# Performance work log

Measured on AMD Instinct MI355X. Metric: run time of the kernel, lower is better.

## Reference

```python
import jax, jax.numpy as jnp
import numpy as np

B, S, D = 4, 4096, 2048
H, DH = 16, 128
ROPE_BASE = 10000.0


def rotate_half(x):
    x1, x2 = jnp.split(x, 2, axis=-1)
    return jnp.concatenate((-x2, x1), axis=-1)


def rope_cos_sin(seq_len, head_dim, dtype):
    inv_freq = 1.0 / (ROPE_BASE ** (jnp.arange(0, head_dim, 2, dtype=jnp.float32) / head_dim))
    pos = jnp.arange(seq_len, dtype=jnp.float32)
    freqs = pos[:, None] * inv_freq[None, :]          # [S, DH/2]
    emb = jnp.concatenate((freqs, freqs), axis=-1)    # [S, DH]
    return jnp.cos(emb).astype(dtype), jnp.sin(emb).astype(dtype)


def setup_inputs() -> dict:
    key = jax.random.key(0)
    ks = jax.random.split(key, 5)
    scale = 0.02
    return {
        "hidden_states": jax.random.normal(ks[0], (B, S, D), jnp.float32),
        "Wq": jax.random.normal(ks[1], (D, D), jnp.float32) * scale,
        "Wk": jax.random.normal(ks[2], (D, D), jnp.float32) * scale,
        "Wv": jax.random.normal(ks[3], (D, D), jnp.float32) * scale,
        "Wo": jax.random.normal(ks[4], (D, D), jnp.float32) * scale,
    }


def reference(hidden_states, Wq, Wk, Wv, Wo):
    b, s, d = hidden_states.shape
    # QKV projections (nn.Linear stores weight as [out, in] -> x @ W.T)
    def proj(W):
        y = hidden_states @ W.T                       # [B, S, D]
        return y.reshape(b, s, H, DH).transpose(0, 2, 1, 3)  # [B, H, S, DH]
    q, k, v = proj(Wq), proj(Wk), proj(Wv)

    # RoPE (cos/sin broadcast over head dim: unsqueeze_dim=1)
    cos, sin = rope_cos_sin(s, DH, hidden_states.dtype)  # [S, DH]
    cos = cos[None, None]                                # [1, 1, S, DH]
    sin = sin[None, None]
    q = q * cos + rotate_half(q) * sin
    k = k * cos + rotate_half(k) * sin

    # SDPA, non-causal, no mask, eval mode (dropout 0)
    scale = 1.0 / jnp.sqrt(jnp.asarray(DH, hidden_states.dtype))
    scores = jnp.einsum("bhqd,bhkd->bhqk", q, k) * scale
    attn = jax.nn.softmax(scores, axis=-1)
    ctx = jnp.einsum("bhqk,bhkd->bhqd", attn, v)         # [B, H, S, DH]

    ctx = ctx.transpose(0, 2, 1, 3).reshape(b, s, H * DH)
    return ctx @ Wo.T
```

## Files before the change

kernel.cpp:

```cpp
#include <hip/hip_runtime.h>
#include <hip/hip_bf16.h>
#include <math.h>

typedef __attribute__((ext_vector_type(4)))  float f32x4;
typedef __attribute__((ext_vector_type(16))) float f32x16;
typedef __attribute__((ext_vector_type(8)))  short s16x8;
typedef __attribute__((ext_vector_type(4)))  short s16x4;
typedef __attribute__((ext_vector_type(4)))  int   i32x4;

#define DEVI __device__ __forceinline__


DEVI unsigned short f2bf(float x) {
    unsigned int u = __builtin_bit_cast(unsigned int, x);
    u += 0x7fffu + ((u >> 16) & 1u);
    return (unsigned short)(u >> 16);
}

DEVI f32x4 mfma16(s16x8 a, s16x8 b, f32x4 c) {
    return __builtin_amdgcn_mfma_f32_16x16x32_bf16(a, b, c, 0, 0, 0);
}
DEVI f32x16 mfma32(s16x8 a, s16x8 b, f32x16 c) {
    return __builtin_amdgcn_mfma_f32_32x32x16_bf16(a, b, c, 0, 0, 0);
}
DEVI int cvtpk(float lo, float hi) {
    int r; asm("v_cvt_pk_bf16_f32 %0, %1, %2" : "=v"(r) : "v"(lo), "v"(hi)); return r;
}
DEVI void plswap(int& a, int& b) {
    asm volatile("v_permlane32_swap_b32 %0, %1" : "+v"(a), "+v"(b));
}
DEVI void gload16(const void* g, void* l) {
    __builtin_amdgcn_global_load_lds(
        (const __attribute__((address_space(1))) void*)g,
        (__attribute__((address_space(3))) void*)l, 16, 0, 0);
}

__global__ __launch_bounds__(256)
void cvt_kernel(const float* __restrict__ in, unsigned short* __restrict__ out, int n8) {
    int i = blockIdx.x * 256 + threadIdx.x;
    const int stride = gridDim.x * 256;
    for (; i < n8; i += stride) {
        f32x4 a = ((const f32x4*)in)[i * 2];
        f32x4 b = ((const f32x4*)in)[i * 2 + 1];
        s16x8 o;
#pragma unroll
        for (int e = 0; e < 4; ++e) o[e] = (short)f2bf(a[e]);
#pragma unroll
        for (int e = 0; e < 4; ++e) o[4 + e] = (short)f2bf(b[e]);
        *(s16x8*)&out[(size_t)i * 8] = o;
    }
}

__global__ void rope_table_kernel(float* __restrict__ cosb, float* __restrict__ sinb) {
    const int s = blockIdx.x;
    const int i = threadIdx.x;
    const float inv = expf(-(float)i * (9.210340371976184f / 64.0f));
    const float ang = (float)s * inv;
    cosb[s * 64 + i] = cosf(ang);
    sinb[s * 64 + i] = sinf(ang);
}

template <bool AB16, bool WB16, int EPI>
__global__ __launch_bounds__(256, 2)
void gemm_kernel(const void* __restrict__ Ap, const void* __restrict__ Bw,
                 void* __restrict__ Cp, const float* __restrict__ cosb,
                 const float* __restrict__ sinb, float oscale)
{
    constexpr bool GL = AB16 && WB16;
    static_assert(GL || !WB16, "non-GL path stages W as f32");
    constexpr int KD = 2048;
    __shared__ __align__(16) unsigned short smem[GL ? 17408 : 20480];

    const int tid  = threadIdx.x;
    const int lane = tid & 63;
    const int wid  = tid >> 6;
    const int wr   = wid >> 1, wc = wid & 1;
    const int lr   = lane & 15;
    const int lkg  = lane >> 4;
    const int lk   = lkg * 8;
    const int m0   = blockIdx.x * 128;
    const int n0   = blockIdx.y * 128;

    const f32x4 zero4 = {0.f, 0.f, 0.f, 0.f};
    f32x4 acc[4][4];
#pragma unroll
    for (int i = 0; i < 4; ++i)
#pragma unroll
        for (int j = 0; j < 4; ++j) acc[i][j] = zero4;

    const int ncol0 = wc * 32;

    if constexpr (GL) {
        const unsigned short* Ah = (const unsigned short*)Ap;
        const unsigned short* Wh = (const unsigned short*)Bw;
        auto stageG = [&](int kt, int buf) {
            const int k0 = kt * 32;
            unsigned short* Ab = smem + buf * 4096;
            unsigned short* Bb = smem + 8192 + buf * 4096;
#pragma unroll
            for (int i = 0; i < 2; ++i) {
                int flat = i * 256 + tid;
                int r = flat >> 2, c = (flat & 3) * 8;
                gload16(&Ah[(size_t)(m0 + r) * KD + k0 + c], Ab + flat * 8);
                gload16(&Wh[(size_t)(n0 + r) * KD + k0 + c], Bb + flat * 8);
            }
        };
        auto computeG = [&](int buf) {
            const unsigned short* Ab = smem + buf * 4096;
            const unsigned short* Bb = smem + 8192 + buf * 4096;
            s16x8 af[4], bf[4];
#pragma unroll
            for (int mi = 0; mi < 4; ++mi)
                af[mi] = *(const s16x8*)&Ab[(wr * 64 + mi * 16 + lr) * 32 + lk];
#pragma unroll
            for (int nj = 0; nj < 4; ++nj) {
                int nc = ncol0 + (nj & 1) * 16 + (nj >> 1) * 64;
                bf[nj] = *(const s16x8*)&Bb[(nc + lr) * 32 + lk];
            }
#pragma unroll
            for (int mi = 0; mi < 4; ++mi)
#pragma unroll
                for (int nj = 0; nj < 4; ++nj)
                    acc[mi][nj] = mfma16(af[mi], bf[nj], acc[mi][nj]);
        };
        stageG(0, 0);
        __syncthreads();
        for (int kt = 0; kt < 64; ++kt) {
            const int cur = kt & 1;
            if (kt < 63) stageG(kt + 1, cur ^ 1);
            computeG(cur);
            __syncthreads();
        }
    } else {
        unsigned short* const As = smem;
        unsigned short* const Bs = smem + 10240;
        f32x4 aF[4], bF[4];
        s16x8 aH[2];
        const float* Af = (const float*)Ap;
        const unsigned short* Ah = (const unsigned short*)Ap;
        const float* Wf = (const float*)Bw;

        auto stage_load = [&](int kt) {
            const int k0 = kt * 32;
            if constexpr (!AB16) {
#pragma unroll
                for (int i = 0; i < 4; ++i) {
                    int flat = i * 256 + tid;
                    int r = flat >> 3, c = (flat & 7) * 4;
                    aF[i] = *(const f32x4*)&Af[(size_t)(m0 + r) * KD + k0 + c];
                }
            } else {
#pragma unroll
                for (int i = 0; i < 2; ++i) {
                    int flat = i * 256 + tid;
                    int r = flat >> 2, c = (flat & 3) * 8;
                    aH[i] = *(const s16x8*)&Ah[(size_t)(m0 + r) * KD + k0 + c];
                }
            }
#pragma unroll
            for (int i = 0; i < 4; ++i) {
                int flat = i * 256 + tid;
                int r = flat >> 3, c = (flat & 7) * 4;
                bF[i] = *(const f32x4*)&Wf[(size_t)(n0 + r) * KD + k0 + c];
            }
        };
        auto stage_write = [&](int buf) {
            unsigned short* Ab = As + buf * 5120;
            unsigned short* Bb = Bs + buf * 5120;
            if constexpr (!AB16) {
#pragma unroll
                for (int i = 0; i < 4; ++i) {
                    int flat = i * 256 + tid;
                    int r = flat >> 3, c = (flat & 7) * 4;
                    s16x4 v;
#pragma unroll
                    for (int e = 0; e < 4; ++e) v[e] = (short)f2bf(aF[i][e]);
                    *(s16x4*)&Ab[r * 40 + c] = v;
                }
            } else {
#pragma unroll
                for (int i = 0; i < 2; ++i) {
                    int flat = i * 256 + tid;
                    int r = flat >> 2, c = (flat & 3) * 8;
                    *(s16x8*)&Ab[r * 40 + c] = aH[i];
                }
            }
#pragma unroll
            for (int i = 0; i < 4; ++i) {
                int flat = i * 256 + tid;
                int r = flat >> 3, c = (flat & 7) * 4;
                s16x4 v;
#pragma unroll
                for (int e = 0; e < 4; ++e) v[e] = (short)f2bf(bF[i][e]);
                *(s16x4*)&Bb[r * 40 + c] = v;
            }
        };
        auto compute = [&](int buf) {
            const unsigned short* Ab = As + buf * 5120;
            const unsigned short* Bb = Bs + buf * 5120;
            s16x8 af[4], bf[4];
#pragma unroll
            for (int mi = 0; mi < 4; ++mi)
                af[mi] = *(const s16x8*)&Ab[(wr * 64 + mi * 16 + lr) * 40 + lk];
#pragma unroll
            for (int nj = 0; nj < 4; ++nj) {
                int nc = ncol0 + (nj & 1) * 16 + (nj >> 1) * 64;
                bf[nj] = *(const s16x8*)&Bb[(nc + lr) * 40 + lk];
            }
#pragma unroll
            for (int mi = 0; mi < 4; ++mi)
#pragma unroll
                for (int nj = 0; nj < 4; ++nj)
                    acc[mi][nj] = mfma16(af[mi], bf[nj], acc[mi][nj]);
        };
        stage_load(0);
        stage_write(0);
        __syncthreads();
        for (int kt = 0; kt < 64; ++kt) {
            const int cur = kt & 1;
            if (kt < 63) stage_load(kt + 1);
            compute(cur);
            if (kt < 63) stage_write(cur ^ 1);
            __syncthreads();
        }
    }

    if constexpr (EPI == 0) {
        unsigned short* Qb = (unsigned short*)Cp;
        const int h = blockIdx.y;
#pragma unroll
        for (int mi = 0; mi < 4; ++mi) {
#pragma unroll
            for (int reg = 0; reg < 4; ++reg) {
                int mg = m0 + wr * 64 + mi * 16 + lkg * 4 + reg;
                int bb = mg >> 12, s = mg & 4095;
                size_t base = ((size_t)(bb * 16 + h) * 4096 + s) * 128;
#pragma unroll
                for (int nj = 0; nj < 2; ++nj) {
                    int dlo = wc * 32 + nj * 16 + lr;
                    float cv = cosb[s * 64 + dlo];
                    float sv = sinb[s * 64 + dlo];
                    float a  = acc[mi][nj][reg];
                    float b2 = acc[mi][nj + 2][reg];
                    Qb[base + dlo]      = f2bf((a * cv - b2 * sv) * oscale);
                    Qb[base + dlo + 64] = f2bf((b2 * cv + a * sv) * oscale);
                }
            }
        }
    } else if constexpr (EPI == 1) {
        unsigned short* Vt = (unsigned short*)Cp;
        const int h = blockIdx.y;
        unsigned short* Cs = smem;
        __syncthreads();
#pragma unroll
        for (int mi = 0; mi < 4; ++mi)
#pragma unroll
            for (int nj = 0; nj < 4; ++nj) {
                int col = wc * 32 + (nj & 1) * 16 + (nj >> 1) * 64 + lr;
#pragma unroll
                for (int reg = 0; reg < 4; ++reg) {
                    int row = wr * 64 + mi * 16 + lkg * 4 + reg;
                    Cs[row * 136 + col] = f2bf(acc[mi][nj][reg]);
                }
            }
        __syncthreads();
        const int dh = tid >> 1;
        const int sh = (tid & 1) * 64;
        const int bb = m0 >> 12, sbase = m0 & 4095;
        size_t gbase = ((size_t)((bb * 16 + h) * 128 + dh)) * 4096 + sbase + sh;
#pragma unroll
        for (int j0 = 0; j0 < 8; ++j0) {
            s16x8 v;
#pragma unroll
            for (int e = 0; e < 8; ++e)
                v[e] = (short)Cs[(sh + j0 * 8 + e) * 136 + dh];
            *(s16x8*)&Vt[gbase + j0 * 8] = v;
        }
    } else {
        float* Ob = (float*)Cp;
#pragma unroll
        for (int mi = 0; mi < 4; ++mi)
#pragma unroll
            for (int reg = 0; reg < 4; ++reg) {
                int mg = m0 + wr * 64 + mi * 16 + lkg * 4 + reg;
#pragma unroll
                for (int nj = 0; nj < 4; ++nj) {
                    int col = n0 + wc * 32 + (nj & 1) * 16 + (nj >> 1) * 64 + lr;
                    Ob[(size_t)mg * 2048 + col] = acc[mi][nj][reg];
                }
            }
    }
}

__global__ __launch_bounds__(512, 2)
void attn_kernel(const unsigned short* __restrict__ Q,
                 const unsigned short* __restrict__ Kb,
                 const unsigned short* __restrict__ Vt,
                 unsigned short* __restrict__ ctx)
{
    __shared__ __align__(16) char smem[65536];

    const int tid  = threadIdx.x;
    const int lane = tid & 63;
    const int wid  = tid >> 6;
    const int l31  = lane & 31;
    const int h    = lane >> 5;
    const int qt   = blockIdx.x;
    const int bh   = blockIdx.y;

    const size_t kbase  = (size_t)bh * 4096;
    const size_t vtbase = (size_t)bh * 128 * 4096;

    const size_t qrow = kbase + (size_t)qt * 256 + wid * 32 + l31;
    s16x8 qf[8];
#pragma unroll
    for (int ks = 0; ks < 8; ++ks)
        qf[ks] = *(const s16x8*)&Q[qrow * 128 + ks * 16 + h * 8];

    const f32x16 Z16 = {0,0,0,0,0,0,0,0,0,0,0,0,0,0,0,0};
    f32x16 accO[4];
    accO[0] = Z16; accO[1] = Z16; accO[2] = Z16; accO[3] = Z16;
    float m = -1e30f, lsum = 0.f;

    auto stage = [&](int buf, int t) {
        const int kv0 = t * 64;
        char* kdst = smem + buf * 32768;
        char* vdst = kdst + 16384;
#pragma unroll
        for (int c = 0; c < 2; ++c) {
            {
                int r   = wid * 8 + c * 4 + (lane >> 4);
                int col = (lane * 16) & 255;
                int cs  = col ^ ((r & 7) << 4);
                gload16(&Kb[(kbase + kv0 + r) * 128 + (cs >> 1)],
                        kdst + wid * 2048 + c * 1024);
            }
            {
                int r   = wid * 16 + c * 8 + (lane >> 3);
                int col = (lane * 16) & 127;
                int cs  = col ^ ((r & 7) << 4);
                gload16(&Vt[vtbase + (size_t)r * 4096 + kv0 + (cs >> 1)],
                        vdst + wid * 2048 + c * 1024);
            }
        }
    };

    const int swz = (l31 & 7) << 4;

    stage(0, 0);
    __syncthreads();

    for (int t = 0; t < 64; ++t) {
        const int buf = t & 1;
        if (t < 63) stage(buf ^ 1, t + 1);

        const char* kb = smem + buf * 32768;
        const char* vb = kb + 16384;

        f32x16 sc0 = Z16, sc1 = Z16;
        __builtin_amdgcn_s_setprio(1);
#pragma unroll
        for (int ks = 0; ks < 8; ++ks) {
            s16x8 k0 = *(const s16x8*)(kb + ((l31 * 256 + ks * 32 + h * 16) ^ swz));
            s16x8 k1 = *(const s16x8*)(kb + (((l31 + 32) * 256 + ks * 32 + h * 16) ^ swz));
            sc0 = mfma32(k0, qf[ks], sc0);
            sc1 = mfma32(k1, qf[ks], sc1);
        }
        __builtin_amdgcn_s_setprio(0);

        float tmx;
        {
            float tr[16];
#pragma unroll
            for (int i = 0; i < 16; ++i) tr[i] = fmaxf(sc0[i], sc1[i]);
#pragma unroll
            for (int s = 8; s > 0; s >>= 1)
#pragma unroll
                for (int i = 0; i < s; ++i) tr[i] = fmaxf(tr[i], tr[i + s]);
            tmx = tr[0];
        }
        tmx = fmaxf(tmx, __shfl_xor(tmx, 32, 64));

        if (!__all(tmx - m <= 8.0f)) {
            const float mnew = fmaxf(m, tmx);
            const float f = exp2f(m - mnew);
            lsum *= f;
            accO[0] *= f; accO[1] *= f; accO[2] *= f; accO[3] *= f;
            m = mnew;
        }

        float p[32];
#pragma unroll
        for (int i = 0; i < 16; ++i) p[i] = exp2f(sc0[i] - m);
#pragma unroll
        for (int i = 0; i < 16; ++i) p[16 + i] = exp2f(sc1[i] - m);
        float ps;
        {
            float ts[16];
#pragma unroll
            for (int i = 0; i < 16; ++i) ts[i] = p[i] + p[16 + i];
#pragma unroll
            for (int s = 8; s > 0; s >>= 1)
#pragma unroll
                for (int i = 0; i < s; ++i) ts[i] += ts[i + s];
            ps = ts[0];
        }
        ps += __shfl_xor(ps, 32, 64);
        lsum += ps;

        s16x8 pb[4];
#pragma unroll
        for (int g = 0; g < 4; ++g) {
            int a0 = cvtpk(p[g * 8 + 0], p[g * 8 + 1]);
            int a1 = cvtpk(p[g * 8 + 2], p[g * 8 + 3]);
            int b0 = cvtpk(p[g * 8 + 4], p[g * 8 + 5]);
            int b1 = cvtpk(p[g * 8 + 6], p[g * 8 + 7]);
            plswap(a0, b0); plswap(a1, b1);
            i32x4 w = {a0, a1, b0, b1};
            pb[g] = __builtin_bit_cast(s16x8, w);
        }

        __builtin_amdgcn_s_setprio(1);
#pragma unroll
        for (int mf = 0; mf < 4; ++mf) {
            const int rowb = (mf * 32 + l31) * 128;
#pragma unroll
            for (int ks = 0; ks < 4; ++ks) {
                s16x8 vf = *(const s16x8*)(vb + ((rowb + ks * 32 + h * 16) ^ swz));
                accO[mf] = mfma32(vf, pb[ks], accO[mf]);
            }
        }
        __builtin_amdgcn_s_setprio(0);

        __syncthreads();
    }

    const float invl = 1.0f / lsum;
    accO[0] *= invl; accO[1] *= invl; accO[2] *= invl; accO[3] *= invl;

    unsigned short* tw = (unsigned short*)smem + wid * 1088;
    const int bb = bh >> 4, hh = bh & 15;
    const size_t cbase = ((size_t)(bb * 4096 + qt * 256 + wid * 32 + l31)) * 2048 + hh * 128;
#pragma unroll
    for (int mf = 0; mf < 4; ++mf) {
#pragma unroll
        for (int reg = 0; reg < 16; ++reg) {
            int d = (reg & 3) + 8 * (reg >> 2) + 4 * h;
            tw[d * 34 + l31] = f2bf(accO[mf][reg]);
        }
        s16x8 o0, o1;
#pragma unroll
        for (int dd = 0; dd < 8; ++dd) {
            o0[dd] = (short)tw[(h * 16 + dd) * 34 + l31];
            o1[dd] = (short)tw[(h * 16 + 8 + dd) * 34 + l31];
        }
        *(s16x8*)&ctx[cbase + mf * 32 + h * 16]     = o0;
        *(s16x8*)&ctx[cbase + mf * 32 + h * 16 + 8] = o1;
    }
}

extern "C" void kernel_launch(void* const* d_in, const int* in_sizes, int n_in,
                              void* d_out, int out_size, void* d_ws, size_t ws_size,
                              hipStream_t stream)
{
    (void)in_sizes; (void)n_in; (void)out_size;
    const float* X  = (const float*)d_in[0];
    const float* Wq = (const float*)d_in[1];
    const float* Wk = (const float*)d_in[2];
    const float* Wv = (const float*)d_in[3];
    const float* Wo = (const float*)d_in[4];

    char* ws = (char*)d_ws;
    const size_t TBL  = 2097152;
    const size_t HBUF = 67108864;
    const size_t WBUF = 8388608;
    const size_t SX   = 33554432;
    const size_t SW   = 4194304;

    float* cosb = (float*)ws;
    float* sinb = (float*)(ws + 1048576);

    const float QSCALE = 0.12751763f;
    dim3 gg(128, 16), blk(256);

    rope_table_kernel<<<dim3(4096), dim3(64), 0, stream>>>(cosb, sinb);

    if (ws_size >= TBL + HBUF + 4 * WBUF + 4 * HBUF) {
        unsigned short* Xb  = (unsigned short*)(ws + TBL);
        unsigned short* Wb0 = (unsigned short*)(ws + TBL + HBUF);
        unsigned short* Qb  = (unsigned short*)(ws + TBL + HBUF + 4 * WBUF);
        unsigned short* Kb  = Qb + SX;
        unsigned short* Vtb = Kb + SX;
        unsigned short* Cb  = Vtb + SX;
        const float* Wsrc[4] = {Wq, Wk, Wv, Wo};
        cvt_kernel<<<dim3(2048), blk, 0, stream>>>(X, Xb, (int)(SX / 8));
        for (int w = 0; w < 4; ++w)
            cvt_kernel<<<dim3(1024), blk, 0, stream>>>(Wsrc[w], Wb0 + w * SW, (int)(SW / 8));
        gemm_kernel<true, true, 0><<<gg, blk, 0, stream>>>(Xb, Wb0,          Qb, cosb, sinb, QSCALE);
        gemm_kernel<true, true, 0><<<gg, blk, 0, stream>>>(Xb, Wb0 + SW,     Kb, cosb, sinb, 1.0f);
        gemm_kernel<true, true, 1><<<gg, blk, 0, stream>>>(Xb, Wb0 + 2 * SW, Vtb, cosb, sinb, 1.0f);
        attn_kernel<<<dim3(16, 64), dim3(512), 0, stream>>>(Qb, Kb, Vtb, Cb);
        gemm_kernel<true, true, 2><<<gg, blk, 0, stream>>>(Cb, Wb0 + 3 * SW, d_out, cosb, sinb, 1.0f);
    } else if (ws_size >= TBL + HBUF + 4 * WBUF + HBUF) {
        unsigned short* Xb  = (unsigned short*)(ws + TBL);
        unsigned short* Wb0 = (unsigned short*)(ws + TBL + HBUF);
        unsigned short* Vtb = (unsigned short*)(ws + TBL + HBUF + 4 * WBUF);
        unsigned short* Qb  = (unsigned short*)d_out;
        unsigned short* Kb  = Qb + SX;
        unsigned short* Cb  = Xb;
        const float* Wsrc[4] = {Wq, Wk, Wv, Wo};
        cvt_kernel<<<dim3(2048), blk, 0, stream>>>(X, Xb, (int)(SX / 8));
        for (int w = 0; w < 4; ++w)
            cvt_kernel<<<dim3(1024), blk, 0, stream>>>(Wsrc[w], Wb0 + w * SW, (int)(SW / 8));
        gemm_kernel<true, true, 0><<<gg, blk, 0, stream>>>(Xb, Wb0,          Qb, cosb, sinb, QSCALE);
        gemm_kernel<true, true, 0><<<gg, blk, 0, stream>>>(Xb, Wb0 + SW,     Kb, cosb, sinb, 1.0f);
        gemm_kernel<true, true, 1><<<gg, blk, 0, stream>>>(Xb, Wb0 + 2 * SW, Vtb, cosb, sinb, 1.0f);
        attn_kernel<<<dim3(16, 64), dim3(512), 0, stream>>>(Qb, Kb, Vtb, Cb);
        gemm_kernel<true, true, 2><<<gg, blk, 0, stream>>>(Cb, Wb0 + 3 * SW, d_out, cosb, sinb, 1.0f);
    } else {
        unsigned short* Vtb = (unsigned short*)(ws + TBL);
        unsigned short* Cb  = (unsigned short*)(ws + TBL + HBUF);
        unsigned short* Qb  = (unsigned short*)d_out;
        unsigned short* Kb  = Qb + SX;
        gemm_kernel<false, false, 0><<<gg, blk, 0, stream>>>(X, Wq, Qb, cosb, sinb, QSCALE);
        gemm_kernel<false, false, 0><<<gg, blk, 0, stream>>>(X, Wk, Kb, cosb, sinb, 1.0f);
        gemm_kernel<false, false, 1><<<gg, blk, 0, stream>>>(X, Wv, Vtb, cosb, sinb, 1.0f);
        attn_kernel<<<dim3(16, 64), dim3(512), 0, stream>>>(Qb, Kb, Vtb, Cb);
        gemm_kernel<true, false, 2><<<gg, blk, 0, stream>>>(Cb, Wo, d_out, cosb, sinb, 1.0f);
    }
}
```

Measured before the change: 1.430 ms.

## Double attention KV tile to 128 and compute row sums with MFMA

The attention kernel now processes 128 keys per iteration instead of 64, with double-buffered K/V tiles, so shared memory grows to 128 KB and the loop runs half as many times with half as many barriers. The softmax row sum is no longer reduced with VALU adds and shuffles. It is accumulated by an extra MFMA against a vector of bf16 ones. The larger LDS footprint likely allows only one 512-thread block per CU despite launch_bounds(512,2), which cuts occupancy and the overlap between waves. The MFMA row sum also adds matrix work and is taken over bf16-rounded probabilities.

After: 1.877 ms. 31.3% more time.

```diff
diff --git a/kernel.cpp b/kernel.cpp
--- a/kernel.cpp
+++ b/kernel.cpp
@@ -298,7 +298,7 @@
                  const unsigned short* __restrict__ Vt,
                  unsigned short* __restrict__ ctx)
 {
-    __shared__ __align__(16) char smem[65536];
+    __shared__ __align__(16) char smem[131072];
 
     const int tid  = threadIdx.x;
     const int lane = tid & 63;
@@ -317,31 +317,28 @@
     for (int ks = 0; ks < 8; ++ks)
         qf[ks] = *(const s16x8*)&Q[qrow * 128 + ks * 16 + h * 8];
 
+    s16x8 ones;
+#pragma unroll
+    for (int e = 0; e < 8; ++e) ones[e] = (short)0x3F80;
+
     const f32x16 Z16 = {0,0,0,0,0,0,0,0,0,0,0,0,0,0,0,0};
     f32x16 accO[4];
     accO[0] = Z16; accO[1] = Z16; accO[2] = Z16; accO[3] = Z16;
-    float m = -1e30f, lsum = 0.f;
+    f32x16 accL = Z16;
+    float m = -1e30f;
 
     auto stage = [&](int buf, int t) {
-        const int kv0 = t * 64;
-        char* kdst = smem + buf * 32768;
-        char* vdst = kdst + 16384;
-#pragma unroll
-        for (int c = 0; c < 2; ++c) {
-            {
-                int r   = wid * 8 + c * 4 + (lane >> 4);
-                int col = (lane * 16) & 255;
-                int cs  = col ^ ((r & 7) << 4);
-                gload16(&Kb[(kbase + kv0 + r) * 128 + (cs >> 1)],
-                        kdst + wid * 2048 + c * 1024);
-            }
-            {
-                int r   = wid * 16 + c * 8 + (lane >> 3);
-                int col = (lane * 16) & 127;
-                int cs  = col ^ ((r & 7) << 4);
-                gload16(&Vt[vtbase + (size_t)r * 4096 + kv0 + (cs >> 1)],
-                        vdst + wid * 2048 + c * 1024);
-            }
+        const int kv0 = t * 128;
+        char* kdst = smem + buf * 65536;
+        char* vdst = kdst + 32768;
+#pragma unroll
+        for (int c = 0; c < 4; ++c) {
+            int flat = c * 512 + tid;
+            int r    = flat >> 4;
+            int col  = (flat & 15) * 16;
+            int cs   = col ^ ((r & 7) << 4);
+            gload16(&Kb[(kbase + kv0 + r) * 128 + (cs >> 1)], kdst + flat * 16);
+            gload16(&Vt[vtbase + (size_t)r * 4096 + kv0 + (cs >> 1)], vdst + flat * 16);
         }
     };
 
@@ -350,21 +347,23 @@
     stage(0, 0);
     __syncthreads();
 
-    for (int t = 0; t < 64; ++t) {
+    for (int t = 0; t < 32; ++t) {
         const int buf = t & 1;
-        if (t < 63) stage(buf ^ 1, t + 1);
-
-        const char* kb = smem + buf * 32768;
-        const char* vb = kb + 16384;
-
-        f32x16 sc0 = Z16, sc1 = Z16;
+        if (t < 31) stage(buf ^ 1, t + 1);
+
+        const char* kb = smem + buf * 65536;
+        const char* vb = kb + 32768;
+
+        f32x16 sc[4];
+        sc[0] = Z16; sc[1] = Z16; sc[2] = Z16; sc[3] = Z16;
         __builtin_amdgcn_s_setprio(1);
 #pragma unroll
         for (int ks = 0; ks < 8; ++ks) {
-            s16x8 k0 = *(const s16x8*)(kb + ((l31 * 256 + ks * 32 + h * 16) ^ swz));
-            s16x8 k1 = *(const s16x8*)(kb + (((l31 + 32) * 256 + ks * 32 + h * 16) ^ swz));
-            sc0 = mfma32(k0, qf[ks], sc0);
-            sc1 = mfma32(k1, qf[ks], sc1);
+#pragma unroll
+            for (int b = 0; b < 4; ++b) {
+                s16x8 kf = *(const s16x8*)(kb + (((b * 32 + l31) * 256 + ks * 32 + h * 16) ^ swz));
+                sc[b] = mfma32(kf, qf[ks], sc[b]);
+            }
         }
         __builtin_amdgcn_s_setprio(0);
 
@@ -372,49 +371,38 @@
         {
             float tr[16];
 #pragma unroll
-            for (int i = 0; i < 16; ++i) tr[i] = fmaxf(sc0[i], sc1[i]);
-#pragma unroll
-            for (int s = 8; s > 0; s >>= 1)
-#pragma unroll
-                for (int i = 0; i < s; ++i) tr[i] = fmaxf(tr[i], tr[i + s]);
-            tmx = tr[0];
+            for (int i = 0; i < 16; ++i)
+                tr[i] = fmaxf(fmaxf(sc[0][i], sc[1][i]), fmaxf(sc[2][i], sc[3][i]));
+#pragma unroll
+            for (int i = 0; i < 5; ++i)
+                tr[i] = fmaxf(fmaxf(tr[i], tr[i + 5]), tr[i + 10]);
+            tr[0] = fmaxf(fmaxf(tr[0], tr[1]), fmaxf(tr[2], tr[15]));
+            tmx = fmaxf(tr[0], fmaxf(tr[3], tr[4]));
         }
         tmx = fmaxf(tmx, __shfl_xor(tmx, 32, 64));
 
         if (!__all(tmx - m <= 8.0f)) {
             const float mnew = fmaxf(m, tmx);
             const float f = exp2f(m - mnew);
-            lsum *= f;
+            accL[0] *= f;
             accO[0] *= f; accO[1] *= f; accO[2] *= f; accO[3] *= f;
             m = mnew;
         }
 
-        float p[32];
-#pragma unroll
-        for (int i = 0; i < 16; ++i) p[i] = exp2f(sc0[i] - m);
-#pragma unroll
-        for (int i = 0; i < 16; ++i) p[16 + i] = exp2f(sc1[i] - m);
-        float ps;
-        {
-            float ts[16];
-#pragma unroll
-            for (int i = 0; i < 16; ++i) ts[i] = p[i] + p[16 + i];
-#pragma unroll
-            for (int s = 8; s > 0; s >>= 1)
-#pragma unroll
-                for (int i = 0; i < s; ++i) ts[i] += ts[i + s];
-            ps = ts[0];
-        }
-        ps += __shfl_xor(ps, 32, 64);
-        lsum += ps;
-
-        s16x8 pb[4];
-#pragma unroll
-        for (int g = 0; g < 4; ++g) {
-            int a0 = cvtpk(p[g * 8 + 0], p[g * 8 + 1]);
-            int a1 = cvtpk(p[g * 8 + 2], p[g * 8 + 3]);
-            int b0 = cvtpk(p[g * 8 + 4], p[g * 8 + 5]);
-            int b1 = cvtpk(p[g * 8 + 6], p[g * 8 + 7]);
+#pragma unroll
+        for (int b = 0; b < 4; ++b)
+#pragma unroll
+            for (int i = 0; i < 16; ++i)
+                sc[b][i] = exp2f(sc[b][i] - m);
+
+        s16x8 pb[8];
+#pragma unroll
+        for (int g = 0; g < 8; ++g) {
+            const int b = g >> 1, o = (g & 1) * 8;
+            int a0 = cvtpk(sc[b][o + 0], sc[b][o + 1]);
+            int a1 = cvtpk(sc[b][o + 2], sc[b][o + 3]);
+            int b0 = cvtpk(sc[b][o + 4], sc[b][o + 5]);
+            int b1 = cvtpk(sc[b][o + 6], sc[b][o + 7]);
             plswap(a0, b0); plswap(a1, b1);
             i32x4 w = {a0, a1, b0, b1};
             pb[g] = __builtin_bit_cast(s16x8, w);
@@ -422,11 +410,11 @@
 
         __builtin_amdgcn_s_setprio(1);
 #pragma unroll
-        for (int mf = 0; mf < 4; ++mf) {
-            const int rowb = (mf * 32 + l31) * 128;
-#pragma unroll
-            for (int ks = 0; ks < 4; ++ks) {
-                s16x8 vf = *(const s16x8*)(vb + ((rowb + ks * 32 + h * 16) ^ swz));
+        for (int ks = 0; ks < 8; ++ks) {
+            accL = mfma32(ones, pb[ks], accL);
+#pragma unroll
+            for (int mf = 0; mf < 4; ++mf) {
+                s16x8 vf = *(const s16x8*)(vb + ((((mf * 32 + l31) * 256) + ks * 32 + h * 16) ^ swz));
                 accO[mf] = mfma32(vf, pb[ks], accO[mf]);
             }
         }
@@ -435,7 +423,7 @@
         __syncthreads();
     }
 
-    const float invl = 1.0f / lsum;
+    const float invl = 1.0f / accL[0];
     accO[0] *= invl; accO[1] *= invl; accO[2] *= invl; accO[3] *= invl;
 
     unsigned short* tw = (unsigned short*)smem + wid * 1088;
```
